# Kernel optimization log

Measured on AMD Instinct MI355X. Metric: run time of the kernel, lower is better.

Reference implementation:

```python
import jax, jax.numpy as jnp
import numpy as np

N = 100_000      # nodes
E = 1_600_000    # edges
D_IN = 128       # input_dim
H = 128          # hidden_dim
L = 3            # num_layers
G = 128          # graphs in batch
EPS = 1e-5       # BatchNorm1d eps


def setup_inputs() -> dict:
    key = jax.random.key(0)
    ks = jax.random.split(key, 8)
    inp = {
        "x": jax.random.normal(ks[0], (N, D_IN), dtype=jnp.float32),
        "edge_index": jax.random.randint(ks[1], (2, E), 0, N),
        "batch": jnp.sort(jax.random.randint(ks[2], (N,), 0, G)),
    }
    for i in range(L):
        din = D_IN if i == 0 else H
        kw = jax.random.fold_in(key, 100 + i)
        inp[f"W{i}"] = jax.random.normal(kw, (din, H), dtype=jnp.float32) / np.sqrt(din).astype(np.float32)
        inp[f"b{i}"] = jnp.zeros((H,), jnp.float32)
        inp[f"g{i}"] = jnp.ones((H,), jnp.float32)
        inp[f"beta{i}"] = jnp.zeros((H,), jnp.float32)
    return inp


def _gcn_conv(x, W, b, src, dst, dinv):
    # GCNConv (normalize=True, add_self_loops=True):
    # out = D^{-1/2} (A + I) D^{-1/2} X W + b, deg computed on dst with self-loops
    h = x @ W                                   # [N,H]
    coef = (dinv[src] * dinv[dst])[:, None]     # per-edge norm
    agg = jax.ops.segment_sum(h[src] * coef, dst, num_segments=N)
    agg = agg + h * (dinv * dinv)[:, None]      # self-loop term deg^{-1}
    return agg + b


def _batchnorm(z, g, beta):
    mu = jnp.mean(z, axis=0)
    var = jnp.mean(jnp.square(z - mu), axis=0)  # biased var (training-mode BN)
    return (z - mu) * jax.lax.rsqrt(var + EPS) * g + beta


def reference(x, edge_index, batch,
              W0, b0, g0, beta0,
              W1, b1, g1, beta1,
              W2, b2, g2, beta2):
    src, dst = edge_index[0], edge_index[1]
    # degree of A + I on target index
    deg = jax.ops.segment_sum(jnp.ones((E,), x.dtype), dst, num_segments=N) + 1.0
    dinv = jax.lax.rsqrt(deg)
    params = [(W0, b0, g0, beta0), (W1, b1, g1, beta1), (W2, b2, g2, beta2)]
    zs = []
    h = x
    for (W, b, g, beta) in params:
        h = _gcn_conv(h, W, b, src, dst, dinv)
        h = jax.nn.relu(h)
        h = _batchnorm(h, g, beta)
        zs.append(h)
    pooled = [jax.ops.segment_sum(z, batch, num_segments=G) for z in zs]  # sum pool
    h_cat = jnp.concatenate(zs, axis=1)        # [N, L*H]
    g_cat = jnp.concatenate(pooled, axis=1)    # [G, L*H]
    return h_cat, g_cat
```

## Files before the change

kernel.cpp:

```cpp
#include <hip/hip_runtime.h>

#define NN 100000
#define NE 1600000
#define NG 128
#define BN_EPS 1e-5f
#define NBKT 64
#define AGG_BLOCKS 2048
#define AGG_WAVES (AGG_BLOCKS * 4)
#define NBUCK 98
#define BIN_BLOCKS 256
#define BIN_CHUNK 6250

typedef short s16x8 __attribute__((ext_vector_type(8)));
typedef float f32x4 __attribute__((ext_vector_type(4)));

static __device__ __forceinline__ unsigned short f2bf(float f) {
    unsigned u = __float_as_uint(f);
    u += 0x7fffu + ((u >> 16) & 1u);
    return (unsigned short)(u >> 16);
}
static __device__ __forceinline__ unsigned packbf(float a, float b) {
    return (unsigned)f2bf(a) | ((unsigned)f2bf(b) << 16);
}
static __device__ __forceinline__ float bf_lo(unsigned u) { return __uint_as_float(u << 16); }
static __device__ __forceinline__ float bf_hi(unsigned u) { return __uint_as_float(u & 0xffff0000u); }
static __device__ __forceinline__ float bf2f(ushort u) { return __uint_as_float((unsigned)u << 16); }

__global__ __launch_bounds__(256) void k_bhist(const int* __restrict__ dst, int* __restrict__ gbh) {
    __shared__ int lh[128];
    int t = threadIdx.x;
    if (t < 128) lh[t] = 0;
    __syncthreads();
    for (int e = blockIdx.x * 256 + t; e < NE; e += gridDim.x * 256)
        atomicAdd(&lh[dst[e] >> 10], 1);
    __syncthreads();
    if (t < 128 && lh[t]) atomicAdd(&gbh[t], lh[t]);
}

__global__ __launch_bounds__(128) void k_bscan(const int* __restrict__ gbh, int* __restrict__ gbase,
                                               int* __restrict__ gcur, int* __restrict__ row_start) {
    __shared__ int s[128];
    int t = threadIdx.x;
    int v = gbh[t];
    s[t] = v;
    __syncthreads();
    for (int o = 1; o < 128; o <<= 1) {
        int a = (t >= o) ? s[t - o] : 0;
        __syncthreads();
        s[t] += a;
        __syncthreads();
    }
    int ex = s[t] - v;
    gbase[t] = ex;
    gcur[t] = ex;
    if (t == 127) { gbase[128] = s[127]; row_start[NN] = NE; }
}

__global__ __launch_bounds__(256) void k_bin(const int* __restrict__ src, const int* __restrict__ dst,
                                             int* __restrict__ gcur, int* __restrict__ tmp) {
    __shared__ int lh[128], lb[128], lc[128];
    int t = threadIdx.x;
    if (t < 128) lh[t] = 0;
    __syncthreads();
    int e0 = blockIdx.x * BIN_CHUNK, e1 = e0 + BIN_CHUNK;
    for (int e = e0 + t; e < e1; e += 256) atomicAdd(&lh[dst[e] >> 10], 1);
    __syncthreads();
    if (t < 128) {
        int c = lh[t];
        lb[t] = c ? atomicAdd(&gcur[t], c) : 0;
        lc[t] = 0;
    }
    __syncthreads();
    for (int e = e0 + t; e < e1; e += 256) {
        int d = dst[e];
        int b = d >> 10;
        int off = atomicAdd(&lc[b], 1);
        tmp[lb[b] + off] = (src[e] << 10) | (d & 1023);
    }
}

__global__ __launch_bounds__(256) void k_csr(const int* __restrict__ tmp, const int* __restrict__ gbase,
                                             int* __restrict__ esrc, int* __restrict__ row_start,
                                             float* __restrict__ dinv) {
    __shared__ int h[1024], hs[1024], part[256];
    int b = blockIdx.x, t = threadIdx.x;
    int base = gbase[b], end = gbase[b + 1];
#pragma unroll
    for (int k = 0; k < 4; ++k) h[t * 4 + k] = 0;
    __syncthreads();
    for (int i = base + t; i < end; i += 256) atomicAdd(&h[tmp[i] & 1023], 1);
    __syncthreads();
    int l0 = h[t * 4], l1 = h[t * 4 + 1], l2 = h[t * 4 + 2], l3 = h[t * 4 + 3];
    int ssum = l0 + l1 + l2 + l3;
    part[t] = ssum;
    __syncthreads();
    for (int o = 1; o < 256; o <<= 1) {
        int a = (t >= o) ? part[t - o] : 0;
        __syncthreads();
        part[t] += a;
        __syncthreads();
    }
    int ex = part[t] - ssum;
    hs[t * 4]     = ex;
    hs[t * 4 + 1] = ex + l0;
    hs[t * 4 + 2] = ex + l0 + l1;
    hs[t * 4 + 3] = ex + l0 + l1 + l2;
    int n0 = b * 1024 + t * 4;
#pragma unroll
    for (int k = 0; k < 4; ++k) {
        int n = n0 + k;
        if (n < NN) {
            row_start[n] = base + hs[t * 4 + k];
            dinv[n] = rsqrtf((float)h[t * 4 + k] + 1.0f);
        }
    }
    __syncthreads();
    for (int i = base + t; i < end; i += 256) {
        int rec = tmp[i];
        int pos = atomicAdd(&hs[rec & 1023], 1);
        esrc[base + pos] = rec >> 10;
    }
}

__global__ __launch_bounds__(64) void k_wfrag(const float* __restrict__ W0, const float* __restrict__ W1,
                                              const float* __restrict__ W2, ushort* __restrict__ Wf) {
    int layer = blockIdx.x >> 5;
    int unit = blockIdx.x & 31;
    const float* W = (layer == 0) ? W0 : ((layer == 1) ? W1 : W2);
    int lane = threadIdx.x;
    int ks = unit >> 3, nb = unit & 7;
    int n = nb * 16 + (lane & 15);
    int k0 = ks * 32 + (lane >> 4) * 8;
    ushort o[8];
#pragma unroll
    for (int j = 0; j < 8; ++j) o[j] = f2bf(W[(size_t)(k0 + j) * 128 + n]);
    ushort* p = Wf + (size_t)layer * 16384 + ((size_t)unit * 64 + lane) * 8;
#pragma unroll
    for (int j = 0; j < 8; ++j) p[j] = o[j];
}

__global__ __launch_bounds__(128) void k_finwscale(const float* __restrict__ S, const float* __restrict__ Q,
                                                   const float* __restrict__ gam, const float* __restrict__ bet,
                                                   float* __restrict__ svec, float* __restrict__ tvec,
                                                   const float* __restrict__ Wnext, float* __restrict__ tW,
                                                   const ushort* __restrict__ Wfb, ushort* __restrict__ Wff) {
    int bid = blockIdx.x;
    int t = threadIdx.x;
    if (bid == 0) {
        __shared__ float ts[128];
        float s = 0.f, q = 0.f;
        for (int k = 0; k < NBKT; ++k) {
            s += S[k * 128 + t];
            q += Q[k * 128 + t];
        }
        float mean = s / (float)NN;
        float var = q / (float)NN - mean * mean;
        float rstd = rsqrtf(fmaxf(var, 0.f) + BN_EPS);
        float sc = gam[t] * rstd;
        float sh = bet[t] - mean * sc;
        svec[t] = sc;
        tvec[t] = sh;
        ts[t] = sh;
        __syncthreads();
        if (Wnext) {
            float acc = 0.f;
            for (int k = 0; k < 128; ++k) acc += ts[k] * Wnext[(size_t)k * 128 + t];
            tW[t] = acc;
        }
    } else {
        __shared__ float sv[32];
        int unit = bid - 1;
        int kbase = (unit >> 3) * 32;
        if (t < 32) {
            int c = kbase + t;
            float s = 0.f, q = 0.f;
            for (int k = 0; k < NBKT; ++k) {
                s += S[k * 128 + c];
                q += Q[k * 128 + c];
            }
            float mean = s / (float)NN;
            float var = q / (float)NN - mean * mean;
            sv[t] = gam[c] * rsqrtf(fmaxf(var, 0.f) + BN_EPS);
        }
        __syncthreads();
        if (t < 64) {
            int ko = (t >> 4) * 8;
            const ushort* p = Wfb + ((size_t)unit * 64 + t) * 8;
            ushort* o = Wff + ((size_t)unit * 64 + t) * 8;
#pragma unroll
            for (int j = 0; j < 8; ++j) o[j] = f2bf(bf2f(p[j]) * sv[ko + j]);
        }
    }
}

__global__ __launch_bounds__(256) void k_gemm(const ushort* __restrict__ Xb, const float* __restrict__ xf32,
                                              const ushort* __restrict__ Wf, const float* __restrict__ tW,
                                              const float* __restrict__ dinv, ushort* __restrict__ hm) {
    int tid = threadIdx.x;
    int wid = tid >> 6, lane = tid & 63;
    int r0 = blockIdx.x * 64 + wid * 16;
    int m = lane & 15, g = lane >> 4;
    int xrow = r0 + m;
    int xr = (xrow < NN) ? xrow : (NN - 1);
    s16x8 af[4];
    if (xf32) {
        const float* Xr = xf32 + (size_t)xr * 128 + g * 8;
#pragma unroll
        for (int ks = 0; ks < 4; ++ks) {
            float4 a = *(const float4*)(Xr + ks * 32);
            float4 b = *(const float4*)(Xr + ks * 32 + 4);
            s16x8 v;
            v[0] = (short)f2bf(a.x); v[1] = (short)f2bf(a.y);
            v[2] = (short)f2bf(a.z); v[3] = (short)f2bf(a.w);
            v[4] = (short)f2bf(b.x); v[5] = (short)f2bf(b.y);
            v[6] = (short)f2bf(b.z); v[7] = (short)f2bf(b.w);
            af[ks] = v;
        }
    } else {
        const ushort* Xrow = Xb + (size_t)xr * 128 + g * 8;
#pragma unroll
        for (int ks = 0; ks < 4; ++ks) af[ks] = *(const s16x8*)(Xrow + ks * 32);
    }
    f32x4 acc[8];
#pragma unroll
    for (int nb = 0; nb < 8; ++nb) acc[nb] = (f32x4){0.f, 0.f, 0.f, 0.f};
#pragma unroll
    for (int ks = 0; ks < 4; ++ks) {
#pragma unroll
        for (int nb = 0; nb < 8; ++nb) {
            s16x8 wf = *(const s16x8*)(Wf + ((size_t)(ks * 8 + nb) * 64 + lane) * 8);
            acc[nb] = __builtin_amdgcn_mfma_f32_16x16x32_bf16(wf, af[ks], acc[nb], 0, 0, 0);
        }
    }
    if (xrow < NN) {
        float ds = dinv[xr];
        ushort* orow = hm + (size_t)xrow * 128 + g * 4;
        if (tW) {
#pragma unroll
            for (int nb = 0; nb < 8; ++nb) {
                float4 tw = *(const float4*)(tW + nb * 16 + g * 4);
                ushort4 o;
                o.x = f2bf(ds * (acc[nb][0] + tw.x));
                o.y = f2bf(ds * (acc[nb][1] + tw.y));
                o.z = f2bf(ds * (acc[nb][2] + tw.z));
                o.w = f2bf(ds * (acc[nb][3] + tw.w));
                *(ushort4*)(orow + nb * 16) = o;
            }
        } else {
#pragma unroll
            for (int nb = 0; nb < 8; ++nb) {
                ushort4 o;
                o.x = f2bf(ds * acc[nb][0]);
                o.y = f2bf(ds * acc[nb][1]);
                o.z = f2bf(ds * acc[nb][2]);
                o.w = f2bf(ds * acc[nb][3]);
                *(ushort4*)(orow + nb * 16) = o;
            }
        }
    }
}

__global__ __launch_bounds__(256) void k_agg(const uint* __restrict__ hm32, const int* __restrict__ esrc,
                                             const int* __restrict__ rs, const float* __restrict__ dinv,
                                             const float* __restrict__ bias, uint* __restrict__ act,
                                             float* __restrict__ bnsum, float* __restrict__ bnsq) {
    __shared__ float ls[128], lq[128];
    int tid = threadIdx.x;
    if (tid < 128) { ls[tid] = 0.f; lq[tid] = 0.f; }
    __syncthreads();
    int lane = tid & 63;
    int wgid = blockIdx.x * 4 + (tid >> 6);
    float2 b2 = *(const float2*)(bias + lane * 2);
    float s0 = 0.f, s1 = 0.f, q0 = 0.f, q1 = 0.f;

    for (int n = wgid; n < NN; n += AGG_WAVES) {
        uint self = hm32[(size_t)n * 64 + lane];
        float a0 = bf_lo(self);
        float a1 = bf_hi(self);

        int i  = __builtin_amdgcn_readfirstlane(rs[n]);
        int i1 = __builtin_amdgcn_readfirstlane(rs[n + 1]);

        int idxv = 0;
        if (i < i1) idxv = esrc[i + min(min(lane, 15), i1 - i - 1)];

        while (i < i1) {
            int cnt = i1 - i;
            cnt = (cnt > 16) ? 16 : cnt;
            int cur = idxv;
            int inext = i + cnt;
            if (inext < i1)
                idxv = esrc[inext + min(min(lane, 15), i1 - inext - 1)];
            uint g[16];
#pragma unroll
            for (int u = 0; u < 16; ++u) {
                int sidx = __builtin_amdgcn_readlane(cur, u);
                sidx = (u < cnt) ? sidx : NN;
                g[u] = hm32[(size_t)sidx * 64 + lane];
            }
#pragma unroll
            for (int u = 0; u < 16; ++u) {
                a0 += bf_lo(g[u]);
                a1 += bf_hi(g[u]);
            }
            i = inext;
        }
        float di = dinv[n];
        float z0 = fmaxf(fmaf(di, a0, b2.x), 0.f);
        float z1 = fmaxf(fmaf(di, a1, b2.y), 0.f);
        act[(size_t)n * 64 + lane] = packbf(z0, z1);
        s0 += z0; s1 += z1;
        q0 += z0 * z0; q1 += z1 * z1;
    }
    atomicAdd(&ls[lane * 2],     s0);
    atomicAdd(&ls[lane * 2 + 1], s1);
    atomicAdd(&lq[lane * 2],     q0);
    atomicAdd(&lq[lane * 2 + 1], q1);
    __syncthreads();
    if (tid < 128) {
        int bkt = blockIdx.x & (NBKT - 1);
        atomicAdd(&bnsum[bkt * 128 + tid], ls[tid]);
        atomicAdd(&bnsq[bkt * 128 + tid],  lq[tid]);
    }
}

__global__ __launch_bounds__(128) void k_pool(const uint* __restrict__ act32, const float* __restrict__ svec,
                                              const float* __restrict__ tvec, const int* __restrict__ batch,
                                              float* __restrict__ gout, float* __restrict__ outp, int lofs) {
    int t = threadIdx.x;
    int lane = t & 63;
    int w = t >> 6;
    int n0 = blockIdx.x * 64;
    float sc0 = svec[lane * 2], sc1 = svec[lane * 2 + 1];
    float sh0 = tvec[lane * 2], sh1 = tvec[lane * 2 + 1];
    float s0 = 0.f, s1 = 0.f;
    int cnt = 0, curg = -1;
    for (int k = w; k < 64; k += 2) {
        int n = n0 + k;
        if (n >= NN) break;
        int gn = batch[n];
        if (gn != curg) {
            if (cnt) {
                atomicAdd(&gout[(size_t)curg * 384 + lofs + lane * 2],     sc0 * s0 + sh0 * (float)cnt);
                atomicAdd(&gout[(size_t)curg * 384 + lofs + lane * 2 + 1], sc1 * s1 + sh1 * (float)cnt);
            }
            curg = gn; s0 = 0.f; s1 = 0.f; cnt = 0;
        }
        uint v = act32[(size_t)n * 64 + lane];
        float a0 = bf_lo(v), a1 = bf_hi(v);
        float2 z;
        z.x = a0 * sc0 + sh0;
        z.y = a1 * sc1 + sh1;
        *(float2*)(outp + (size_t)n * 384 + lofs + lane * 2) = z;
        s0 += a0;
        s1 += a1;
        ++cnt;
    }
    if (cnt) {
        atomicAdd(&gout[(size_t)curg * 384 + lofs + lane * 2],     sc0 * s0 + sh0 * (float)cnt);
        atomicAdd(&gout[(size_t)curg * 384 + lofs + lane * 2 + 1], sc1 * s1 + sh1 * (float)cnt);
    }
}

extern "C" void kernel_launch(void* const* d_in, const int* in_sizes, int n_in,
                              void* d_out, int out_size, void* d_ws, size_t ws_size,
                              hipStream_t stream) {
    const float* x = (const float*)d_in[0];
    const int* ei = (const int*)d_in[1];
    const int* src = ei;
    const int* dst = ei + NE;
    const int* batch = (const int*)d_in[2];
    const float *W[3], *b[3], *g[3], *beta[3];
    for (int l = 0; l < 3; ++l) {
        W[l]    = (const float*)d_in[3 + 4 * l];
        b[l]    = (const float*)d_in[4 + 4 * l];
        g[l]    = (const float*)d_in[5 + 4 * l];
        beta[l] = (const float*)d_in[6 + 4 * l];
    }
    float* out = (float*)d_out;
    float* gout = out + (size_t)NN * 384;

    char* ws = (char*)d_ws;
    size_t off = 0;
    auto alloc = [&](size_t bytes) -> char* {
        off = (off + 255) & ~(size_t)255;
        char* p = ws + off;
        off += bytes;
        return p;
    };
    ushort* act      = (ushort*)alloc((size_t)NN * 256);
    ushort* hm       = (ushort*)alloc((size_t)(NN + 1) * 256);
    int*    esrc     = (int*)alloc((size_t)NE * 4);
    int*    tmp      = (int*)alloc((size_t)NE * 4);
    int*    row_start= (int*)alloc((size_t)(NN + 1) * 4);
    float*  dinv     = (float*)alloc((size_t)NN * 4);
    float*  bnst     = (float*)alloc((size_t)3 * 2 * NBKT * 128 * 4);
    ushort* Wf       = (ushort*)alloc(3 * 16384 * 2);
    ushort* Wff      = (ushort*)alloc(16384 * 2);
    float*  svt      = (float*)alloc(3 * 2 * 128 * 4);
    float*  tW       = (float*)alloc(128 * 4);
    int*    misc     = (int*)alloc(512 * 4);
    int* gbh   = misc;
    int* gbase = misc + 128;
    int* gcur  = misc + 384;
    (void)ws_size;

    hipMemsetAsync(gbh, 0, 128 * 4, stream);
    hipMemsetAsync(hm + (size_t)NN * 128, 0, 256, stream);
    hipMemsetAsync(bnst, 0, (size_t)3 * 2 * NBKT * 128 * 4, stream);
    hipMemsetAsync(gout, 0, (size_t)NG * 384 * 4, stream);

    k_bhist<<<512, 256, 0, stream>>>(dst, gbh);
    k_bscan<<<1, 128, 0, stream>>>(gbh, gbase, gcur, row_start);
    k_bin<<<BIN_BLOCKS, 256, 0, stream>>>(src, dst, gcur, tmp);
    k_csr<<<NBUCK, 256, 0, stream>>>(tmp, gbase, esrc, row_start, dinv);
    k_wfrag<<<96, 64, 0, stream>>>(W[0], W[1], W[2], Wf);

    for (int l = 0; l < 3; ++l) {
        float* S = bnst + (size_t)l * 2 * NBKT * 128;
        float* Q = S + NBKT * 128;
        float* sv = svt + l * 256;
        float* tv = sv + 128;
        const ushort* gin = (l == 0) ? (const ushort*)nullptr : act;
        const float* xin = (l == 0) ? x : nullptr;
        const ushort* wfrag = (l == 0) ? (Wf + 0) : Wff;
        const float* tw_in = (l == 0) ? nullptr : tW;

        k_gemm<<<(NN + 63) / 64, 256, 0, stream>>>(gin, xin, wfrag, tw_in, dinv, hm);
        k_agg<<<AGG_BLOCKS, 256, 0, stream>>>((const uint*)hm, esrc, row_start, dinv, b[l],
                                              (uint*)act, S, Q);
        k_finwscale<<<(l < 2) ? 33 : 1, 128, 0, stream>>>(S, Q, g[l], beta[l], sv, tv,
                                                          (l < 2) ? W[l + 1] : nullptr, tW,
                                                          (l < 2) ? (Wf + (l + 1) * 16384) : nullptr, Wff);
        k_pool<<<(NN + 63) / 64, 128, 0, stream>>>((const uint*)act, sv, tv, batch, gout, out, l * 128);
    }
}
```

Baseline: 460.9 us.

## Fuse graph build and per-layer agg/BN/pool into cooperative grid-sync kernels

```diff
diff --git a/kernel.cpp b/kernel.cpp
--- a/kernel.cpp
+++ b/kernel.cpp
@@ -1,15 +1,17 @@
 #include <hip/hip_runtime.h>
+#include <hip/hip_cooperative_groups.h>
+
+namespace cg = cooperative_groups;
 
 #define NN 100000
 #define NE 1600000
 #define NG 128
 #define BN_EPS 1e-5f
 #define NBKT 64
-#define AGG_BLOCKS 2048
-#define AGG_WAVES (AGG_BLOCKS * 4)
 #define NBUCK 98
 #define BIN_BLOCKS 256
 #define BIN_CHUNK 6250
+#define POOL_CHUNKS 1563
 
 typedef short s16x8 __attribute__((ext_vector_type(8)));
 typedef float f32x4 __attribute__((ext_vector_type(4)));
@@ -26,43 +28,42 @@
 static __device__ __forceinline__ float bf_hi(unsigned u) { return __uint_as_float(u & 0xffff0000u); }
 static __device__ __forceinline__ float bf2f(ushort u) { return __uint_as_float((unsigned)u << 16); }
 
-__global__ __launch_bounds__(256) void k_bhist(const int* __restrict__ dst, int* __restrict__ gbh) {
-    __shared__ int lh[128];
-    int t = threadIdx.x;
+
+__device__ __forceinline__ void dev_bhist(const int* __restrict__ dst, int* __restrict__ gbh,
+                                          int* lh, int b, int nb, int t) {
     if (t < 128) lh[t] = 0;
     __syncthreads();
-    for (int e = blockIdx.x * 256 + t; e < NE; e += gridDim.x * 256)
-        atomicAdd(&lh[dst[e] >> 10], 1);
+    for (int e = b * 256 + t; e < NE; e += nb * 256) atomicAdd(&lh[dst[e] >> 10], 1);
     __syncthreads();
     if (t < 128 && lh[t]) atomicAdd(&gbh[t], lh[t]);
 }
 
-__global__ __launch_bounds__(128) void k_bscan(const int* __restrict__ gbh, int* __restrict__ gbase,
-                                               int* __restrict__ gcur, int* __restrict__ row_start) {
-    __shared__ int s[128];
-    int t = threadIdx.x;
-    int v = gbh[t];
-    s[t] = v;
+__device__ __forceinline__ void dev_bscan(const int* __restrict__ gbh, int* __restrict__ gbase,
+                                          int* __restrict__ gcur, int* __restrict__ row_start,
+                                          int* sbuf, int t) {
+    int v = (t < 128) ? gbh[t] : 0;
+    sbuf[t] = v;
     __syncthreads();
     for (int o = 1; o < 128; o <<= 1) {
-        int a = (t >= o) ? s[t - o] : 0;
+        int a = (t >= o && t < 128) ? sbuf[t - o] : 0;
         __syncthreads();
-        s[t] += a;
+        sbuf[t] += a;
         __syncthreads();
     }
-    int ex = s[t] - v;
-    gbase[t] = ex;
-    gcur[t] = ex;
-    if (t == 127) { gbase[128] = s[127]; row_start[NN] = NE; }
-}
-
-__global__ __launch_bounds__(256) void k_bin(const int* __restrict__ src, const int* __restrict__ dst,
-                                             int* __restrict__ gcur, int* __restrict__ tmp) {
-    __shared__ int lh[128], lb[128], lc[128];
-    int t = threadIdx.x;
+    if (t < 128) {
+        int ex = sbuf[t] - v;
+        gbase[t] = ex;
+        gcur[t] = ex;
+        if (t == 127) { gbase[128] = sbuf[127]; row_start[NN] = NE; }
+    }
+}
+
+__device__ __forceinline__ void dev_bin(const int* __restrict__ src, const int* __restrict__ dst,
+                                        int* __restrict__ gcur, int* __restrict__ tmp,
+                                        int* lh, int* lb, int* lc, int chunk, int t) {
     if (t < 128) lh[t] = 0;
     __syncthreads();
-    int e0 = blockIdx.x * BIN_CHUNK, e1 = e0 + BIN_CHUNK;
+    int e0 = chunk * BIN_CHUNK, e1 = e0 + BIN_CHUNK;
     for (int e = e0 + t; e < e1; e += 256) atomicAdd(&lh[dst[e] >> 10], 1);
     __syncthreads();
     if (t < 128) {
@@ -73,18 +74,18 @@
     __syncthreads();
     for (int e = e0 + t; e < e1; e += 256) {
         int d = dst[e];
-        int b = d >> 10;
-        int off = atomicAdd(&lc[b], 1);
-        tmp[lb[b] + off] = (src[e] << 10) | (d & 1023);
-    }
-}
-
-__global__ __launch_bounds__(256) void k_csr(const int* __restrict__ tmp, const int* __restrict__ gbase,
-                                             int* __restrict__ esrc, int* __restrict__ row_start,
-                                             float* __restrict__ dinv) {
-    __shared__ int h[1024], hs[1024], part[256];
-    int b = blockIdx.x, t = threadIdx.x;
-    int base = gbase[b], end = gbase[b + 1];
+        int bb = d >> 10;
+        int off = atomicAdd(&lc[bb], 1);
+        tmp[lb[bb] + off] = (src[e] << 10) | (d & 1023);
+    }
+    __syncthreads();
+}
+
+__device__ __forceinline__ void dev_csr(const int* __restrict__ tmp, const int* __restrict__ gbase,
+                                        int* __restrict__ esrc, int* __restrict__ row_start,
+                                        float* __restrict__ dinv, int* h, int* hs, int* part,
+                                        int bk, int t) {
+    int base = gbase[bk], end = gbase[bk + 1];
 #pragma unroll
     for (int k = 0; k < 4; ++k) h[t * 4 + k] = 0;
     __syncthreads();
@@ -105,7 +106,7 @@
     hs[t * 4 + 1] = ex + l0;
     hs[t * 4 + 2] = ex + l0 + l1;
     hs[t * 4 + 3] = ex + l0 + l1 + l2;
-    int n0 = b * 1024 + t * 4;
+    int n0 = bk * 1024 + t * 4;
 #pragma unroll
     for (int k = 0; k < 4; ++k) {
         int n = n0 + k;
@@ -120,56 +121,114 @@
         int pos = atomicAdd(&hs[rec & 1023], 1);
         esrc[base + pos] = rec >> 10;
     }
-}
-
-__global__ __launch_bounds__(64) void k_wfrag(const float* __restrict__ W0, const float* __restrict__ W1,
-                                              const float* __restrict__ W2, ushort* __restrict__ Wf) {
-    int layer = blockIdx.x >> 5;
-    int unit = blockIdx.x & 31;
-    const float* W = (layer == 0) ? W0 : ((layer == 1) ? W1 : W2);
-    int lane = threadIdx.x;
+    __syncthreads();
+}
+
+__device__ __forceinline__ void dev_wfrag(const float* __restrict__ W, ushort* __restrict__ Wfl,
+                                          int unit, int t) {
+    if (t >= 64) return;
     int ks = unit >> 3, nb = unit & 7;
-    int n = nb * 16 + (lane & 15);
-    int k0 = ks * 32 + (lane >> 4) * 8;
+    int n = nb * 16 + (t & 15);
+    int k0 = ks * 32 + (t >> 4) * 8;
     ushort o[8];
 #pragma unroll
     for (int j = 0; j < 8; ++j) o[j] = f2bf(W[(size_t)(k0 + j) * 128 + n]);
-    ushort* p = Wf + (size_t)layer * 16384 + ((size_t)unit * 64 + lane) * 8;
+    ushort* p = Wfl + ((size_t)unit * 64 + t) * 8;
 #pragma unroll
     for (int j = 0; j < 8; ++j) p[j] = o[j];
 }
 
-__global__ __launch_bounds__(128) void k_finwscale(const float* __restrict__ S, const float* __restrict__ Q,
-                                                   const float* __restrict__ gam, const float* __restrict__ bet,
-                                                   float* __restrict__ svec, float* __restrict__ tvec,
-                                                   const float* __restrict__ Wnext, float* __restrict__ tW,
-                                                   const ushort* __restrict__ Wfb, ushort* __restrict__ Wff) {
-    int bid = blockIdx.x;
-    int t = threadIdx.x;
-    if (bid == 0) {
-        __shared__ float ts[128];
-        float s = 0.f, q = 0.f;
-        for (int k = 0; k < NBKT; ++k) {
-            s += S[k * 128 + t];
-            q += Q[k * 128 + t];
-        }
-        float mean = s / (float)NN;
-        float var = q / (float)NN - mean * mean;
-        float rstd = rsqrtf(fmaxf(var, 0.f) + BN_EPS);
-        float sc = gam[t] * rstd;
-        float sh = bet[t] - mean * sc;
-        svec[t] = sc;
-        tvec[t] = sh;
-        ts[t] = sh;
+__device__ __forceinline__ void dev_agg(const uint* __restrict__ hm32, const int* __restrict__ esrc,
+                                        const int* __restrict__ rs, const float* __restrict__ dinv,
+                                        const float* __restrict__ bias, uint* __restrict__ act,
+                                        float* __restrict__ bnsum, float* __restrict__ bnsq,
+                                        float* ls, float* lq, int tid, int wgid, int nwaves, int bkt) {
+    if (tid < 128) { ls[tid] = 0.f; lq[tid] = 0.f; }
+    __syncthreads();
+    int lane = tid & 63;
+    float2 b2 = *(const float2*)(bias + lane * 2);
+    float s0 = 0.f, s1 = 0.f, q0 = 0.f, q1 = 0.f;
+
+    for (int n = wgid; n < NN; n += nwaves) {
+        uint self = hm32[(size_t)n * 64 + lane];
+        float a0 = bf_lo(self);
+        float a1 = bf_hi(self);
+
+        int i  = __builtin_amdgcn_readfirstlane(rs[n]);
+        int i1 = __builtin_amdgcn_readfirstlane(rs[n + 1]);
+
+        int idxv = 0;
+        if (i < i1) idxv = esrc[i + min(min(lane, 15), i1 - i - 1)];
+
+        while (i < i1) {
+            int cnt = i1 - i;
+            cnt = (cnt > 16) ? 16 : cnt;
+            int cur = idxv;
+            int inext = i + cnt;
+            if (inext < i1)
+                idxv = esrc[inext + min(min(lane, 15), i1 - inext - 1)];
+            uint g[16];
+#pragma unroll
+            for (int u = 0; u < 16; ++u) {
+                int sidx = __builtin_amdgcn_readlane(cur, u);
+                sidx = (u < cnt) ? sidx : NN;
+                g[u] = hm32[(size_t)sidx * 64 + lane];
+            }
+#pragma unroll
+            for (int u = 0; u < 16; ++u) {
+                a0 += bf_lo(g[u]);
+                a1 += bf_hi(g[u]);
+            }
+            i = inext;
+        }
+        float di = dinv[n];
+        float z0 = fmaxf(fmaf(di, a0, b2.x), 0.f);
+        float z1 = fmaxf(fmaf(di, a1, b2.y), 0.f);
+        act[(size_t)n * 64 + lane] = packbf(z0, z1);
+        s0 += z0; s1 += z1;
+        q0 += z0 * z0; q1 += z1 * z1;
+    }
+    atomicAdd(&ls[lane * 2],     s0);
+    atomicAdd(&ls[lane * 2 + 1], s1);
+    atomicAdd(&lq[lane * 2],     q0);
+    atomicAdd(&lq[lane * 2 + 1], q1);
+    __syncthreads();
+    if (tid < 128) {
+        atomicAdd(&bnsum[bkt * 128 + tid], ls[tid]);
+        atomicAdd(&bnsq[bkt * 128 + tid],  lq[tid]);
+    }
+}
+
+__device__ __forceinline__ void dev_finw(const float* __restrict__ S, const float* __restrict__ Q,
+                                         const float* __restrict__ gam, const float* __restrict__ bet,
+                                         float* __restrict__ svec, float* __restrict__ tvec,
+                                         const float* __restrict__ Wnext, float* __restrict__ tW,
+                                         const ushort* __restrict__ Wfb, ushort* __restrict__ Wff,
+                                         float* ts, float* svl, int b, int t) {
+    if (b == 0) {
+        if (t < 128) {
+            float s = 0.f, q = 0.f;
+            for (int k = 0; k < NBKT; ++k) {
+                s += S[k * 128 + t];
+                q += Q[k * 128 + t];
+            }
+            float mean = s / (float)NN;
+            float var = q / (float)NN - mean * mean;
+            float rstd = rsqrtf(fmaxf(var, 0.f) + BN_EPS);
+            float sc = gam[t] * rstd;
+            float sh = bet[t] - mean * sc;
+            svec[t] = sc;
+            tvec[t] = sh;
+            ts[t] = sh;
+        }
         __syncthreads();
-        if (Wnext) {
+        if (Wnext && t < 128) {
             float acc = 0.f;
             for (int k = 0; k < 128; ++k) acc += ts[k] * Wnext[(size_t)k * 128 + t];
             tW[t] = acc;
         }
-    } else {
-        __shared__ float sv[32];
-        int unit = bid - 1;
+    } else if (b <= 32 && Wfb) {
+        int unit = b - 1;
         int kbase = (unit >> 3) * 32;
         if (t < 32) {
             int c = kbase + t;
@@ -180,7 +239,7 @@
             }
             float mean = s / (float)NN;
             float var = q / (float)NN - mean * mean;
-            sv[t] = gam[c] * rsqrtf(fmaxf(var, 0.f) + BN_EPS);
+            svl[t] = gam[c] * rsqrtf(fmaxf(var, 0.f) + BN_EPS);
         }
         __syncthreads();
         if (t < 64) {
@@ -188,9 +247,158 @@
             const ushort* p = Wfb + ((size_t)unit * 64 + t) * 8;
             ushort* o = Wff + ((size_t)unit * 64 + t) * 8;
 #pragma unroll
-            for (int j = 0; j < 8; ++j) o[j] = f2bf(bf2f(p[j]) * sv[ko + j]);
-        }
-    }
+            for (int j = 0; j < 8; ++j) o[j] = f2bf(bf2f(p[j]) * svl[ko + j]);
+        }
+    }
+}
+
+__device__ __forceinline__ void dev_pool(const uint* __restrict__ act32, const float* __restrict__ svec,
+                                         const float* __restrict__ tvec, const int* __restrict__ batch,
+                                         float* __restrict__ gout, float* __restrict__ outp, int lofs,
+                                         int nb0, int nbstride, int tid) {
+    int lane = tid & 63;
+    int w = tid >> 6;
+    float sc0 = svec[lane * 2], sc1 = svec[lane * 2 + 1];
+    float sh0 = tvec[lane * 2], sh1 = tvec[lane * 2 + 1];
+    for (int nb = nb0; nb < POOL_CHUNKS; nb += nbstride) {
+        int n0 = nb * 64;
+        float s0 = 0.f, s1 = 0.f;
+        int cnt = 0, curg = -1;
+        for (int k = w; k < 64; k += 4) {
+            int n = n0 + k;
+            if (n >= NN) break;
+            int gn = batch[n];
+            if (gn != curg) {
+                if (cnt) {
+                    atomicAdd(&gout[(size_t)curg * 384 + lofs + lane * 2],     sc0 * s0 + sh0 * (float)cnt);
+                    atomicAdd(&gout[(size_t)curg * 384 + lofs + lane * 2 + 1], sc1 * s1 + sh1 * (float)cnt);
+                }
+                curg = gn; s0 = 0.f; s1 = 0.f; cnt = 0;
+            }
+            uint v = act32[(size_t)n * 64 + lane];
+            float a0 = bf_lo(v), a1 = bf_hi(v);
+            float2 z;
+            z.x = a0 * sc0 + sh0;
+            z.y = a1 * sc1 + sh1;
+            *(float2*)(outp + (size_t)n * 384 + lofs + lane * 2) = z;
+            s0 += a0;
+            s1 += a1;
+            ++cnt;
+        }
+        if (cnt) {
+            atomicAdd(&gout[(size_t)curg * 384 + lofs + lane * 2],     sc0 * s0 + sh0 * (float)cnt);
+            atomicAdd(&gout[(size_t)curg * 384 + lofs + lane * 2 + 1], sc1 * s1 + sh1 * (float)cnt);
+        }
+    }
+}
+
+
+__global__ __launch_bounds__(256) void k_build(const float* __restrict__ W0, const float* __restrict__ W1,
+                                               const float* __restrict__ W2, const int* __restrict__ src,
+                                               const int* __restrict__ dst, ushort* __restrict__ Wf,
+                                               int* __restrict__ gbh, int* __restrict__ gbase,
+                                               int* __restrict__ gcur, int* __restrict__ row_start,
+                                               int* __restrict__ tmp, int* __restrict__ esrc,
+                                               float* __restrict__ dinv, float* __restrict__ bnst,
+                                               float* __restrict__ gout, uint* __restrict__ hmz) {
+    cg::grid_group grid = cg::this_grid();
+    __shared__ int lh[128], lb[128], lc[128];
+    __shared__ int h[1024], hs[1024], part[256];
+    int t = threadIdx.x, b = blockIdx.x;
+    int nb = gridDim.x;
+
+    if (b < 96) {
+        int layer = b >> 5, unit = b & 31;
+        const float* W = (layer == 0) ? W0 : ((layer == 1) ? W1 : W2);
+        dev_wfrag(W, Wf + (size_t)layer * 16384, unit, t);
+    } else {
+        int gid = (b - 96) * 256 + t;
+        if (gid < 128) gbh[gid] = 0;
+        else if (gid < 49280) bnst[gid - 128] = 0.f;
+        else if (gid < 98432) gout[gid - 49280] = 0.f;
+        else if (gid < 98496) hmz[gid - 98432] = 0u;
+    }
+    grid.sync();
+    dev_bhist(dst, gbh, lh, b, nb, t);
+    grid.sync();
+    if (b == 0) dev_bscan(gbh, gbase, gcur, row_start, part, t);
+    grid.sync();
+    for (int c = b; c < BIN_BLOCKS; c += nb) dev_bin(src, dst, gcur, tmp, lh, lb, lc, c, t);
+    grid.sync();
+    for (int bk = b; bk < NBUCK; bk += nb) dev_csr(tmp, gbase, esrc, row_start, dinv, h, hs, part, bk, t);
+}
+
+__global__ __launch_bounds__(256) void k_layer(const uint* __restrict__ hm32, const int* __restrict__ esrc,
+                                               const int* __restrict__ rs, const float* __restrict__ dinv,
+                                               const float* __restrict__ bias, uint* __restrict__ act,
+                                               float* __restrict__ S, float* __restrict__ Q,
+                                               const float* __restrict__ gam, const float* __restrict__ bet,
+                                               float* __restrict__ svec, float* __restrict__ tvec,
+                                               const float* __restrict__ Wnext, float* __restrict__ tW,
+                                               const ushort* __restrict__ Wfb, ushort* __restrict__ Wff,
+                                               const int* __restrict__ batch, float* __restrict__ gout,
+                                               float* __restrict__ outp, int lofs) {
+    cg::grid_group grid = cg::this_grid();
+    __shared__ float ls[128], lq[128];
+    __shared__ float ts[128], svl[32];
+    int tid = threadIdx.x;
+    int wgid = blockIdx.x * 4 + (tid >> 6);
+    dev_agg(hm32, esrc, rs, dinv, bias, act, S, Q, ls, lq, tid, wgid, gridDim.x * 4,
+            blockIdx.x & (NBKT - 1));
+    grid.sync();
+    dev_finw(S, Q, gam, bet, svec, tvec, Wnext, tW, Wfb, Wff, ts, svl, blockIdx.x, tid);
+    grid.sync();
+    dev_pool(act, svec, tvec, batch, gout, outp, lofs, blockIdx.x, gridDim.x, tid);
+}
+
+
+__global__ __launch_bounds__(256) void k_bhist(const int* __restrict__ dst, int* __restrict__ gbh) {
+    __shared__ int lh[128];
+    dev_bhist(dst, gbh, lh, blockIdx.x, gridDim.x, threadIdx.x);
+}
+__global__ __launch_bounds__(256) void k_bscan(const int* __restrict__ gbh, int* __restrict__ gbase,
+                                               int* __restrict__ gcur, int* __restrict__ row_start) {
+    __shared__ int sbuf[256];
+    dev_bscan(gbh, gbase, gcur, row_start, sbuf, threadIdx.x);
+}
+__global__ __launch_bounds__(256) void k_bin(const int* __restrict__ src, const int* __restrict__ dst,
+                                             int* __restrict__ gcur, int* __restrict__ tmp) {
+    __shared__ int lh[128], lb[128], lc[128];
+    dev_bin(src, dst, gcur, tmp, lh, lb, lc, blockIdx.x, threadIdx.x);
+}
+__global__ __launch_bounds__(256) void k_csr(const int* __restrict__ tmp, const int* __restrict__ gbase,
+                                             int* __restrict__ esrc, int* __restrict__ row_start,
+                                             float* __restrict__ dinv) {
+    __shared__ int h[1024], hs[1024], part[256];
+    dev_csr(tmp, gbase, esrc, row_start, dinv, h, hs, part, blockIdx.x, threadIdx.x);
+}
+__global__ __launch_bounds__(256) void k_wfrag(const float* __restrict__ W0, const float* __restrict__ W1,
+                                               const float* __restrict__ W2, ushort* __restrict__ Wf) {
+    int layer = blockIdx.x >> 5;
+    const float* W = (layer == 0) ? W0 : ((layer == 1) ? W1 : W2);
+    dev_wfrag(W, Wf + (size_t)layer * 16384, blockIdx.x & 31, threadIdx.x);
+}
+__global__ __launch_bounds__(256) void k_agg(const uint* __restrict__ hm32, const int* __restrict__ esrc,
+                                             const int* __restrict__ rs, const float* __restrict__ dinv,
+                                             const float* __restrict__ bias, uint* __restrict__ act,
+                                             float* __restrict__ bnsum, float* __restrict__ bnsq) {
+    __shared__ float ls[128], lq[128];
+    int tid = threadIdx.x;
+    dev_agg(hm32, esrc, rs, dinv, bias, act, bnsum, bnsq, ls, lq, tid,
+            blockIdx.x * 4 + (tid >> 6), gridDim.x * 4, blockIdx.x & (NBKT - 1));
+}
+__global__ __launch_bounds__(256) void k_finwscale(const float* __restrict__ S, const float* __restrict__ Q,
+                                                   const float* __restrict__ gam, const float* __restrict__ bet,
+                                                   float* __restrict__ svec, float* __restrict__ tvec,
+                                                   const float* __restrict__ Wnext, float* __restrict__ tW,
+                                                   const ushort* __restrict__ Wfb, ushort* __restrict__ Wff) {
+    __shared__ float ts[128], svl[32];
+    dev_finw(S, Q, gam, bet, svec, tvec, Wnext, tW, Wfb, Wff, ts, svl, blockIdx.x, threadIdx.x);
+}
+__global__ __launch_bounds__(256) void k_pool(const uint* __restrict__ act32, const float* __restrict__ svec,
+                                              const float* __restrict__ tvec, const int* __restrict__ batch,
+                                              float* __restrict__ gout, float* __restrict__ outp, int lofs) {
+    dev_pool(act32, svec, tvec, batch, gout, outp, lofs, blockIdx.x, gridDim.x, threadIdx.x);
 }
 
 __global__ __launch_bounds__(256) void k_gemm(const ushort* __restrict__ Xb, const float* __restrict__ xf32,
@@ -257,108 +465,6 @@
                 *(ushort4*)(orow + nb * 16) = o;
             }
         }
-    }
-}
-
-__global__ __launch_bounds__(256) void k_agg(const uint* __restrict__ hm32, const int* __restrict__ esrc,
-                                             const int* __restrict__ rs, const float* __restrict__ dinv,
-                                             const float* __restrict__ bias, uint* __restrict__ act,
-                                             float* __restrict__ bnsum, float* __restrict__ bnsq) {
-    __shared__ float ls[128], lq[128];
-    int tid = threadIdx.x;
-    if (tid < 128) { ls[tid] = 0.f; lq[tid] = 0.f; }
-    __syncthreads();
-    int lane = tid & 63;
-    int wgid = blockIdx.x * 4 + (tid >> 6);
-    float2 b2 = *(const float2*)(bias + lane * 2);
-    float s0 = 0.f, s1 = 0.f, q0 = 0.f, q1 = 0.f;
-
-    for (int n = wgid; n < NN; n += AGG_WAVES) {
-        uint self = hm32[(size_t)n * 64 + lane];
-        float a0 = bf_lo(self);
-        float a1 = bf_hi(self);
-
-        int i  = __builtin_amdgcn_readfirstlane(rs[n]);
-        int i1 = __builtin_amdgcn_readfirstlane(rs[n + 1]);
-
-        int idxv = 0;
-        if (i < i1) idxv = esrc[i + min(min(lane, 15), i1 - i - 1)];
-
-        while (i < i1) {
-            int cnt = i1 - i;
-            cnt = (cnt > 16) ? 16 : cnt;
-            int cur = idxv;
-            int inext = i + cnt;
-            if (inext < i1)
-                idxv = esrc[inext + min(min(lane, 15), i1 - inext - 1)];
-            uint g[16];
-#pragma unroll
-            for (int u = 0; u < 16; ++u) {
-                int sidx = __builtin_amdgcn_readlane(cur, u);
-                sidx = (u < cnt) ? sidx : NN;
-                g[u] = hm32[(size_t)sidx * 64 + lane];
-            }
-#pragma unroll
-            for (int u = 0; u < 16; ++u) {
-                a0 += bf_lo(g[u]);
-                a1 += bf_hi(g[u]);
-            }
-            i = inext;
-        }
-        float di = dinv[n];
-        float z0 = fmaxf(fmaf(di, a0, b2.x), 0.f);
-        float z1 = fmaxf(fmaf(di, a1, b2.y), 0.f);
-        act[(size_t)n * 64 + lane] = packbf(z0, z1);
-        s0 += z0; s1 += z1;
-        q0 += z0 * z0; q1 += z1 * z1;
-    }
-    atomicAdd(&ls[lane * 2],     s0);
-    atomicAdd(&ls[lane * 2 + 1], s1);
-    atomicAdd(&lq[lane * 2],     q0);
-    atomicAdd(&lq[lane * 2 + 1], q1);
-    __syncthreads();
-    if (tid < 128) {
-        int bkt = blockIdx.x & (NBKT - 1);
-        atomicAdd(&bnsum[bkt * 128 + tid], ls[tid]);
-        atomicAdd(&bnsq[bkt * 128 + tid],  lq[tid]);
-    }
-}
-
-__global__ __launch_bounds__(128) void k_pool(const uint* __restrict__ act32, const float* __restrict__ svec,
-                                              const float* __restrict__ tvec, const int* __restrict__ batch,
-                                              float* __restrict__ gout, float* __restrict__ outp, int lofs) {
-    int t = threadIdx.x;
-    int lane = t & 63;
-    int w = t >> 6;
-    int n0 = blockIdx.x * 64;
-    float sc0 = svec[lane * 2], sc1 = svec[lane * 2 + 1];
-    float sh0 = tvec[lane * 2], sh1 = tvec[lane * 2 + 1];
-    float s0 = 0.f, s1 = 0.f;
-    int cnt = 0, curg = -1;
-    for (int k = w; k < 64; k += 2) {
-        int n = n0 + k;
-        if (n >= NN) break;
-        int gn = batch[n];
-        if (gn != curg) {
-            if (cnt) {
-                atomicAdd(&gout[(size_t)curg * 384 + lofs + lane * 2],     sc0 * s0 + sh0 * (float)cnt);
-                atomicAdd(&gout[(size_t)curg * 384 + lofs + lane * 2 + 1], sc1 * s1 + sh1 * (float)cnt);
-            }
-            curg = gn; s0 = 0.f; s1 = 0.f; cnt = 0;
-        }
-        uint v = act32[(size_t)n * 64 + lane];
-        float a0 = bf_lo(v), a1 = bf_hi(v);
-        float2 z;
-        z.x = a0 * sc0 + sh0;
-        z.y = a1 * sc1 + sh1;
-        *(float2*)(outp + (size_t)n * 384 + lofs + lane * 2) = z;
-        s0 += a0;
-        s1 += a1;
-        ++cnt;
-    }
-    if (cnt) {
-        atomicAdd(&gout[(size_t)curg * 384 + lofs + lane * 2],     sc0 * s0 + sh0 * (float)cnt);
-        atomicAdd(&gout[(size_t)curg * 384 + lofs + lane * 2 + 1], sc1 * s1 + sh1 * (float)cnt);
     }
 }
 
@@ -403,18 +509,37 @@
     int* gbh   = misc;
     int* gbase = misc + 128;
     int* gcur  = misc + 384;
+    uint* hmz  = (uint*)(hm + (size_t)NN * 128);
     (void)ws_size;
 
-    hipMemsetAsync(gbh, 0, 128 * 4, stream);
-    hipMemsetAsync(hm + (size_t)NN * 128, 0, 256, stream);
-    hipMemsetAsync(bnst, 0, (size_t)3 * 2 * NBKT * 128 * 4, stream);
-    hipMemsetAsync(gout, 0, (size_t)NG * 384 * 4, stream);
-
-    k_bhist<<<512, 256, 0, stream>>>(dst, gbh);
-    k_bscan<<<1, 128, 0, stream>>>(gbh, gbase, gcur, row_start);
-    k_bin<<<BIN_BLOCKS, 256, 0, stream>>>(src, dst, gcur, tmp);
-    k_csr<<<NBUCK, 256, 0, stream>>>(tmp, gbase, esrc, row_start, dinv);
-    k_wfrag<<<96, 64, 0, stream>>>(W[0], W[1], W[2], Wf);
+    {
+        const float* w0 = W[0]; const float* w1 = W[1]; const float* w2 = W[2];
+        const int* sp = src; const int* dp = dst;
+        ushort* wfp = Wf; int* gbhp = gbh; int* gbasep = gbase; int* gcurp = gcur;
+        int* rsp = row_start; int* tmpp = tmp; int* esp = esrc; float* dvp = dinv;
+        float* bnp = bnst; float* gop = gout; uint* hzp = hmz;
+        void* a1[] = {&w0, &w1, &w2, &sp, &dp, &wfp, &gbhp, &gbasep, &gcurp,
+                      &rsp, &tmpp, &esp, &dvp, &bnp, &gop, &hzp};
+        hipError_t e1 = hipLaunchCooperativeKernel((void*)k_build, dim3(512), dim3(256), a1, 0, stream);
+        if (e1 != hipSuccess) {
+            hipMemsetAsync(gbh, 0, 128 * 4, stream);
+            hipMemsetAsync(hmz, 0, 256, stream);
+            hipMemsetAsync(bnst, 0, (size_t)3 * 2 * NBKT * 128 * 4, stream);
+            hipMemsetAsync(gout, 0, (size_t)NG * 384 * 4, stream);
+            k_bhist<<<512, 256, 0, stream>>>(dst, gbh);
+            k_bscan<<<1, 256, 0, stream>>>(gbh, gbase, gcur, row_start);
+            k_bin<<<BIN_BLOCKS, 256, 0, stream>>>(src, dst, gcur, tmp);
+            k_csr<<<NBUCK, 256, 0, stream>>>(tmp, gbase, esrc, row_start, dinv);
+            k_wfrag<<<96, 256, 0, stream>>>(W[0], W[1], W[2], Wf);
+        }
+    }
+
+    int maxb = 0;
+    if (hipOccupancyMaxActiveBlocksPerMultiprocessor(&maxb, k_layer, 256, 0) != hipSuccess || maxb < 1)
+        maxb = 4;
+    int grid2 = maxb * 256;
+    if (grid2 > 2048) grid2 = 2048;
+    if (grid2 < 256) grid2 = 256;
 
     for (int l = 0; l < 3; ++l) {
         float* S = bnst + (size_t)l * 2 * NBKT * 128;
@@ -427,11 +552,32 @@
         const float* tw_in = (l == 0) ? nullptr : tW;
 
         k_gemm<<<(NN + 63) / 64, 256, 0, stream>>>(gin, xin, wfrag, tw_in, dinv, hm);
-        k_agg<<<AGG_BLOCKS, 256, 0, stream>>>((const uint*)hm, esrc, row_start, dinv, b[l],
-                                              (uint*)act, S, Q);
-        k_finwscale<<<(l < 2) ? 33 : 1, 128, 0, stream>>>(S, Q, g[l], beta[l], sv, tv,
-                                                          (l < 2) ? W[l + 1] : nullptr, tW,
-                                                          (l < 2) ? (Wf + (l + 1) * 16384) : nullptr, Wff);
-        k_pool<<<(NN + 63) / 64, 128, 0, stream>>>((const uint*)act, sv, tv, batch, gout, out, l * 128);
-    }
-}
+
+        const uint* hmp = (const uint*)hm;
+        const int* esp = esrc;
+        const int* rsp = row_start;
+        const float* dvp = dinv;
+        const float* bp = b[l];
+        uint* actp = (uint*)act;
+        float* Sp = S; float* Qp = Q;
+        const float* gp = g[l]; const float* bep = beta[l];
+        float* svp = sv; float* tvp = tv;
+        const float* wnp = (l < 2) ? W[l + 1] : nullptr;
+        float* twp = tW;
+        const ushort* wfbp = (l < 2) ? (Wf + (size_t)(l + 1) * 16384) : nullptr;
+        ushort* wffp = Wff;
+        const int* bap = batch;
+        float* gop = gout;
+        float* outp = out;
+        int lofs = l * 128;
+        void* a2[] = {&hmp, &esp, &rsp, &dvp, &bp, &actp, &Sp, &Qp, &gp, &bep,
+                      &svp, &tvp, &wnp, &twp, &wfbp, &wffp, &bap, &gop, &outp, &lofs};
+        hipError_t e2 = hipLaunchCooperativeKernel((void*)k_layer, dim3(grid2), dim3(256), a2, 0, stream);
+        if (e2 != hipSuccess) {
+            k_agg<<<2048, 256, 0, stream>>>(hmp, esrc, row_start, dinv, b[l], (uint*)act, S, Q);
+            k_finwscale<<<(l < 2) ? 33 : 1, 256, 0, stream>>>(S, Q, g[l], beta[l], sv, tv,
+                                                              wnp, tW, wfbp, Wff);
+            k_pool<<<POOL_CHUNKS, 256, 0, stream>>>((const uint*)act, sv, tv, batch, gout, out, lofs);
+        }
+    }
+}
```

After: 1.339 ms. 2.9x slower.

## Fuse setup memsets/wfrag, bucket scan, and BN finalize into last-block epilogues

Applied to the files above, without the earlier changes.

```diff
diff --git a/kernel.cpp b/kernel.cpp
--- a/kernel.cpp
+++ b/kernel.cpp
@@ -26,8 +26,40 @@
 static __device__ __forceinline__ float bf_hi(unsigned u) { return __uint_as_float(u & 0xffff0000u); }
 static __device__ __forceinline__ float bf2f(ushort u) { return __uint_as_float((unsigned)u << 16); }
 
-__global__ __launch_bounds__(256) void k_bhist(const int* __restrict__ dst, int* __restrict__ gbh) {
-    __shared__ int lh[128];
+__global__ __launch_bounds__(256) void k_setup(const float* __restrict__ W0, const float* __restrict__ W1,
+                                               const float* __restrict__ W2, ushort* __restrict__ Wf,
+                                               int* __restrict__ gbh, int* __restrict__ ticks,
+                                               float* __restrict__ bnst, float* __restrict__ gout,
+                                               uint* __restrict__ hmz) {
+    int b = blockIdx.x, t = threadIdx.x;
+    if (b < 96) {
+        if (t >= 64) return;
+        int layer = b >> 5, unit = b & 31;
+        const float* W = (layer == 0) ? W0 : ((layer == 1) ? W1 : W2);
+        int ks = unit >> 3, nb = unit & 7;
+        int n = nb * 16 + (t & 15);
+        int k0 = ks * 32 + (t >> 4) * 8;
+        ushort o[8];
+#pragma unroll
+        for (int j = 0; j < 8; ++j) o[j] = f2bf(W[(size_t)(k0 + j) * 128 + n]);
+        ushort* p = Wf + (size_t)layer * 16384 + ((size_t)unit * 64 + t) * 8;
+#pragma unroll
+        for (int j = 0; j < 8; ++j) p[j] = o[j];
+    } else {
+        int gid = (b - 96) * 256 + t;
+        if (gid < 49152) bnst[gid] = 0.f;
+        else if (gid < 98304) gout[gid - 49152] = 0.f;
+        else if (gid < 98432) gbh[gid - 98304] = 0;
+        else if (gid < 98440) ticks[gid - 98432] = 0;
+        else if (gid < 98504) hmz[gid - 98440] = 0u;
+    }
+}
+
+__global__ __launch_bounds__(256) void k_bhist(const int* __restrict__ dst, int* __restrict__ gbh,
+                                               int* __restrict__ gbase, int* __restrict__ gcur,
+                                               int* __restrict__ row_start, int* __restrict__ tick) {
+    __shared__ int lh[128], sbuf[128];
+    __shared__ int isLast;
     int t = threadIdx.x;
     if (t < 128) lh[t] = 0;
     __syncthreads();
@@ -35,25 +67,26 @@
         atomicAdd(&lh[dst[e] >> 10], 1);
     __syncthreads();
     if (t < 128 && lh[t]) atomicAdd(&gbh[t], lh[t]);
-}
-
-__global__ __launch_bounds__(128) void k_bscan(const int* __restrict__ gbh, int* __restrict__ gbase,
-                                               int* __restrict__ gcur, int* __restrict__ row_start) {
-    __shared__ int s[128];
-    int t = threadIdx.x;
-    int v = gbh[t];
-    s[t] = v;
+    __threadfence();
+    __syncthreads();
+    if (t == 0) isLast = (atomicAdd(tick, 1) == (int)gridDim.x - 1);
+    __syncthreads();
+    if (!isLast) return;
+    int v = 0;
+    if (t < 128) { v = atomicAdd(&gbh[t], 0); sbuf[t] = v; }
     __syncthreads();
     for (int o = 1; o < 128; o <<= 1) {
-        int a = (t >= o) ? s[t - o] : 0;
-        __syncthreads();
-        s[t] += a;
-        __syncthreads();
-    }
-    int ex = s[t] - v;
-    gbase[t] = ex;
-    gcur[t] = ex;
-    if (t == 127) { gbase[128] = s[127]; row_start[NN] = NE; }
+        int a = (t >= o && t < 128) ? sbuf[t - o] : 0;
+        __syncthreads();
+        if (t < 128) sbuf[t] += a;
+        __syncthreads();
+    }
+    if (t < 128) {
+        int ex = sbuf[t] - v;
+        gbase[t] = ex;
+        gcur[t] = ex;
+        if (t == 127) { gbase[128] = sbuf[127]; row_start[NN] = NE; }
+    }
 }
 
 __global__ __launch_bounds__(256) void k_bin(const int* __restrict__ src, const int* __restrict__ dst,
@@ -119,77 +152,6 @@
         int rec = tmp[i];
         int pos = atomicAdd(&hs[rec & 1023], 1);
         esrc[base + pos] = rec >> 10;
-    }
-}
-
-__global__ __launch_bounds__(64) void k_wfrag(const float* __restrict__ W0, const float* __restrict__ W1,
-                                              const float* __restrict__ W2, ushort* __restrict__ Wf) {
-    int layer = blockIdx.x >> 5;
-    int unit = blockIdx.x & 31;
-    const float* W = (layer == 0) ? W0 : ((layer == 1) ? W1 : W2);
-    int lane = threadIdx.x;
-    int ks = unit >> 3, nb = unit & 7;
-    int n = nb * 16 + (lane & 15);
-    int k0 = ks * 32 + (lane >> 4) * 8;
-    ushort o[8];
-#pragma unroll
-    for (int j = 0; j < 8; ++j) o[j] = f2bf(W[(size_t)(k0 + j) * 128 + n]);
-    ushort* p = Wf + (size_t)layer * 16384 + ((size_t)unit * 64 + lane) * 8;
-#pragma unroll
-    for (int j = 0; j < 8; ++j) p[j] = o[j];
-}
-
-__global__ __launch_bounds__(128) void k_finwscale(const float* __restrict__ S, const float* __restrict__ Q,
-                                                   const float* __restrict__ gam, const float* __restrict__ bet,
-                                                   float* __restrict__ svec, float* __restrict__ tvec,
-                                                   const float* __restrict__ Wnext, float* __restrict__ tW,
-                                                   const ushort* __restrict__ Wfb, ushort* __restrict__ Wff) {
-    int bid = blockIdx.x;
-    int t = threadIdx.x;
-    if (bid == 0) {
-        __shared__ float ts[128];
-        float s = 0.f, q = 0.f;
-        for (int k = 0; k < NBKT; ++k) {
-            s += S[k * 128 + t];
-            q += Q[k * 128 + t];
-        }
-        float mean = s / (float)NN;
-        float var = q / (float)NN - mean * mean;
-        float rstd = rsqrtf(fmaxf(var, 0.f) + BN_EPS);
-        float sc = gam[t] * rstd;
-        float sh = bet[t] - mean * sc;
-        svec[t] = sc;
-        tvec[t] = sh;
-        ts[t] = sh;
-        __syncthreads();
-        if (Wnext) {
-            float acc = 0.f;
-            for (int k = 0; k < 128; ++k) acc += ts[k] * Wnext[(size_t)k * 128 + t];
-            tW[t] = acc;
-        }
-    } else {
-        __shared__ float sv[32];
-        int unit = bid - 1;
-        int kbase = (unit >> 3) * 32;
-        if (t < 32) {
-            int c = kbase + t;
-            float s = 0.f, q = 0.f;
-            for (int k = 0; k < NBKT; ++k) {
-                s += S[k * 128 + c];
-                q += Q[k * 128 + c];
-            }
-            float mean = s / (float)NN;
-            float var = q / (float)NN - mean * mean;
-            sv[t] = gam[c] * rsqrtf(fmaxf(var, 0.f) + BN_EPS);
-        }
-        __syncthreads();
-        if (t < 64) {
-            int ko = (t >> 4) * 8;
-            const ushort* p = Wfb + ((size_t)unit * 64 + t) * 8;
-            ushort* o = Wff + ((size_t)unit * 64 + t) * 8;
-#pragma unroll
-            for (int j = 0; j < 8; ++j) o[j] = f2bf(bf2f(p[j]) * sv[ko + j]);
-        }
     }
 }
 
@@ -263,8 +225,14 @@
 __global__ __launch_bounds__(256) void k_agg(const uint* __restrict__ hm32, const int* __restrict__ esrc,
                                              const int* __restrict__ rs, const float* __restrict__ dinv,
                                              const float* __restrict__ bias, uint* __restrict__ act,
-                                             float* __restrict__ bnsum, float* __restrict__ bnsq) {
+                                             float* __restrict__ bnsum, float* __restrict__ bnsq,
+                                             const float* __restrict__ gam, const float* __restrict__ bet,
+                                             float* __restrict__ svec, float* __restrict__ tvec,
+                                             const float* __restrict__ Wnext, float* __restrict__ tW,
+                                             const ushort* __restrict__ Wfb, ushort* __restrict__ Wff,
+                                             int* __restrict__ tick) {
     __shared__ float ls[128], lq[128];
+    __shared__ int isLast;
     int tid = threadIdx.x;
     if (tid < 128) { ls[tid] = 0.f; lq[tid] = 0.f; }
     __syncthreads();
@@ -321,6 +289,53 @@
         int bkt = blockIdx.x & (NBKT - 1);
         atomicAdd(&bnsum[bkt * 128 + tid], ls[tid]);
         atomicAdd(&bnsq[bkt * 128 + tid],  lq[tid]);
+    }
+    __threadfence();
+    __syncthreads();
+    if (tid == 0) isLast = (atomicAdd(tick, 1) == (int)gridDim.x - 1);
+    __syncthreads();
+    if (!isLast) return;
+
+    {
+        int ch = tid & 127, half = tid >> 7;
+        float s = 0.f, q = 0.f;
+#pragma unroll 8
+        for (int k = half * 32; k < half * 32 + 32; ++k) {
+            s += atomicAdd(&bnsum[k * 128 + ch], 0.f);
+            q += atomicAdd(&bnsq[k * 128 + ch], 0.f);
+        }
+        __syncthreads();
+        if (half) { ls[ch] = s; lq[ch] = q; }
+        __syncthreads();
+        if (!half) {
+            s += ls[ch]; q += lq[ch];
+            float mean = s / (float)NN;
+            float var = q / (float)NN - mean * mean;
+            float rstd = rsqrtf(fmaxf(var, 0.f) + BN_EPS);
+            float sc = gam[ch] * rstd;
+            float sh = bet[ch] - mean * sc;
+            svec[ch] = sc;
+            tvec[ch] = sh;
+            ls[ch] = sc;
+            lq[ch] = sh;
+        }
+        __syncthreads();
+        if (Wnext) {
+            if (tid < 128) {
+                float acc = 0.f;
+#pragma unroll 8
+                for (int k = 0; k < 128; ++k) acc += lq[k] * Wnext[(size_t)k * 128 + tid];
+                tW[tid] = acc;
+            }
+            for (int p = tid; p < 2048; p += 256) {
+                int unit = p >> 6, ln = p & 63;
+                int k0 = (unit >> 3) * 32 + ((ln >> 4) & 3) * 8;
+                const ushort* pp = Wfb + ((size_t)unit * 64 + ln) * 8;
+                ushort* oo = Wff + ((size_t)unit * 64 + ln) * 8;
+#pragma unroll
+                for (int j = 0; j < 8; ++j) oo[j] = f2bf(bf2f(pp[j]) * ls[k0 + j]);
+            }
+        }
     }
 }
 
@@ -399,22 +414,18 @@
     ushort* Wff      = (ushort*)alloc(16384 * 2);
     float*  svt      = (float*)alloc(3 * 2 * 128 * 4);
     float*  tW       = (float*)alloc(128 * 4);
-    int*    misc     = (int*)alloc(512 * 4);
+    int*    misc     = (int*)alloc(1024 * 4);
     int* gbh   = misc;
     int* gbase = misc + 128;
     int* gcur  = misc + 384;
+    int* ticks = misc + 512;
+    uint* hmz  = (uint*)(hm + (size_t)NN * 128);
     (void)ws_size;
 
-    hipMemsetAsync(gbh, 0, 128 * 4, stream);
-    hipMemsetAsync(hm + (size_t)NN * 128, 0, 256, stream);
-    hipMemsetAsync(bnst, 0, (size_t)3 * 2 * NBKT * 128 * 4, stream);
-    hipMemsetAsync(gout, 0, (size_t)NG * 384 * 4, stream);
-
-    k_bhist<<<512, 256, 0, stream>>>(dst, gbh);
-    k_bscan<<<1, 128, 0, stream>>>(gbh, gbase, gcur, row_start);
+    k_setup<<<481, 256, 0, stream>>>(W[0], W[1], W[2], Wf, gbh, ticks, bnst, gout, hmz);
+    k_bhist<<<512, 256, 0, stream>>>(dst, gbh, gbase, gcur, row_start, ticks);
     k_bin<<<BIN_BLOCKS, 256, 0, stream>>>(src, dst, gcur, tmp);
     k_csr<<<NBUCK, 256, 0, stream>>>(tmp, gbase, esrc, row_start, dinv);
-    k_wfrag<<<96, 64, 0, stream>>>(W[0], W[1], W[2], Wf);
 
     for (int l = 0; l < 3; ++l) {
         float* S = bnst + (size_t)l * 2 * NBKT * 128;
@@ -425,13 +436,13 @@
         const float* xin = (l == 0) ? x : nullptr;
         const ushort* wfrag = (l == 0) ? (Wf + 0) : Wff;
         const float* tw_in = (l == 0) ? nullptr : tW;
+        const float* wnp = (l < 2) ? W[l + 1] : nullptr;
+        const ushort* wfbp = (l < 2) ? (Wf + (size_t)(l + 1) * 16384) : nullptr;
 
         k_gemm<<<(NN + 63) / 64, 256, 0, stream>>>(gin, xin, wfrag, tw_in, dinv, hm);
         k_agg<<<AGG_BLOCKS, 256, 0, stream>>>((const uint*)hm, esrc, row_start, dinv, b[l],
-                                              (uint*)act, S, Q);
-        k_finwscale<<<(l < 2) ? 33 : 1, 128, 0, stream>>>(S, Q, g[l], beta[l], sv, tv,
-                                                          (l < 2) ? W[l + 1] : nullptr, tW,
-                                                          (l < 2) ? (Wf + (l + 1) * 16384) : nullptr, Wff);
+                                              (uint*)act, S, Q, g[l], beta[l], sv, tv,
+                                              wnp, tW, wfbp, Wff, ticks + 1 + l);
         k_pool<<<(NN + 63) / 64, 128, 0, stream>>>((const uint*)act, sv, tv, batch, gout, out, l * 128);
     }
 }
```

After: 989.6 us. 115% more time.
